# Kernel tuning notes

Measured on AMD Instinct MI355X. Metric: run time of the kernel, lower is better.

## Reference

```python
import jax, jax.numpy as jnp
import numpy as np

H = 8          # multihead_num (also groups of the Conv1d)
LN_EPS = 1e-5  # torch.nn.LayerNorm default


def _gconv(x, w):
    """Grouped Conv1d, kernel=3, stride=1, 'same' reflect padding, no bias.
    x: [B, C_in, L], w: [C_out, C_in//H, K] (torch OIH layout)."""
    xp = jnp.pad(x, ((0, 0), (0, 0), (1, 1)), mode='reflect')
    return jax.lax.conv_general_dilated(
        xp, w, window_strides=(1,), padding='VALID',
        feature_group_count=H, dimension_numbers=('NCH', 'OIH', 'NCH'))


def setup_inputs() -> dict:
    key = jax.random.key(0)
    ks = jax.random.split(key, 5)
    B, C, L = 8, 512, 1024
    q = jax.random.normal(ks[0], (B, C, L), jnp.float32)
    k = jax.random.normal(ks[1], (B, C, L), jnp.float32)
    # causal mask: 1 above the diagonal -> -1e9 subtracted pre-softmax
    mask = jnp.triu(jnp.ones((L, L), jnp.float32), k=1)
    # init_params: std = sqrt(2 / (C_out + C_in/groups))
    std = float(np.sqrt(2.0 / (C + C // H)))
    wq = jax.random.normal(ks[2], (C, C // H, 3), jnp.float32) * std
    wk = jax.random.normal(ks[3], (C, C // H, 3), jnp.float32) * std
    wv = jax.random.normal(ks[4], (C, C // H, 3), jnp.float32) * std
    gamma = jnp.ones((C,), jnp.float32)
    beta = jnp.zeros((C,), jnp.float32)
    return {"q": q, "k": k, "mask": mask, "wq": wq, "wk": wk, "wv": wv,
            "gamma": gamma, "beta": beta}


def reference(q, k, mask, wq, wk, wv, gamma, beta):
    init = q                               # residual branch, [B, C, L]
    B, C, L = q.shape
    D = C // H                             # head dim
    v = k                                  # inputs list of length 2 -> v = k

    qh = _gconv(q, wq).reshape(B, H, D, L)  # split(dim=1)+cat(dim=0) == head axis
    kh = _gconv(k, wk).reshape(B, H, D, L)
    vh = _gconv(v, wv).reshape(B, H, D, L)

    # scores: q^T k per head; NOTE: scaled by sqrt(multihead_num), as in source
    scores = jnp.einsum('bhdl,bhdm->bhlm', qh, kh) / jnp.sqrt(
        jnp.asarray(H, qh.dtype))
    scores = scores - 1e9 * mask           # mask broadcast over [B, H]
    att = jax.nn.softmax(scores, axis=-1)  # dropout p=0.0 -> identity

    # o = att @ v^T, then concat heads along channel (head-major order)
    o = jnp.einsum('bhlm,bhdm->blhd', att, vh).reshape(B, L, C)

    # residual add + LayerNorm over channel dim
    x = o + jnp.swapaxes(init, 1, 2)       # [B, L, C]
    mu = jnp.mean(x, axis=-1, keepdims=True)
    var = jnp.mean(jnp.square(x - mu), axis=-1, keepdims=True)
    y = (x - mu) * jax.lax.rsqrt(var + LN_EPS) * gamma + beta
    return jnp.swapaxes(y, 1, 2)           # [B, C, L]
```

## Files before the change

kernel.cpp:

```cpp
#include <hip/hip_runtime.h>
#include <math.h>

#define H 8
#define B 8
#define C 512
#define L 1024
#define D 64
#define LDK 72

typedef __attribute__((ext_vector_type(4))) float f32x4;
typedef __attribute__((ext_vector_type(8))) short bf16x8;

static __device__ __forceinline__ short f2bf(float x) {
    union { float f; unsigned u; } v; v.f = x;
    unsigned r = v.u + 0x7FFFu + ((v.u >> 16) & 1u);
    return (short)(r >> 16);
}
static __device__ __forceinline__ short f2bf_fast(float x) {
    union { float f; unsigned u; } v; v.f = x;
    return (short)((v.u + 0x8000u) >> 16);
}
static __device__ __forceinline__ int pack2(short a, short b) {
    return (int)((unsigned short)a | ((unsigned)(unsigned short)b << 16));
}
static __device__ __forceinline__ float bfs2f(short v) {
    union { unsigned u; float f; } w; w.u = ((unsigned)(unsigned short)v) << 16;
    return w.f;
}

__global__ __launch_bounds__(256) void wprep_kernel(
    const float* __restrict__ wq, const float* __restrict__ wk,
    const float* __restrict__ wv, short* __restrict__ wtg)
{
    int idx = blockIdx.x * 256 + threadIdx.x;
    int jj    = idx & 7;
    int quad  = (idx >> 3) & 3;
    int d     = (idx >> 5) & 63;
    int r     = idx >> 11;
    int khalf = r & 1;  r >>= 1;
    int t     = r % 3;  r /= 3;
    int h     = r & 7;
    int conv  = r >> 3;
    const float* w = (conv == 0) ? wq : (conv == 1) ? wk : wv;
    int j_in = khalf * 32 + quad * 8 + jj;
    float v = w[(h * 64 + d) * 192 + j_in * 3 + t];
    if (conv == 0) v *= 0.51012254f;
    wtg[idx] = f2bf(v);
}

__global__ __launch_bounds__(256) void conv_kernel(
    const float* __restrict__ q, const float* __restrict__ k,
    const short* __restrict__ wtg,
    short* __restrict__ qh, short* __restrict__ kh, short* __restrict__ vh)
{
    int bx   = blockIdx.x;
    int tile = bx & 15;
    int h    = (bx >> 4) & 7;
    int b    = (bx >> 7) & 7;
    int src  = bx >> 10;

    __shared__ short xT[66 * LDK];

    int l0  = tile * 64;
    int tid = threadIdx.x;
    int wave = tid >> 6, lane = tid & 63;
    int n = lane & 15, quad = lane >> 4;

    const float* x  = src ? k : q;
    const float* xb = x + (size_t)(b * C + h * 64) * L + l0;

    int c0 = src ? 1 : 0;
    const short* wb0 = wtg + (size_t)((c0 * 8 + h) * 3 * 2) * 2048;
    bf16x8 wf[3][2], wf2[3][2];
    #pragma unroll
    for (int t = 0; t < 3; t++)
        #pragma unroll
        for (int kk = 0; kk < 2; kk++)
            wf[t][kk] = *(const bf16x8*)(wb0 + (t * 2 + kk) * 2048
                                         + (wave * 16 + n) * 32 + quad * 8);
    if (src) {
        const short* wb1 = wtg + (size_t)((2 * 8 + h) * 3 * 2) * 2048;
        #pragma unroll
        for (int t = 0; t < 3; t++)
            #pragma unroll
            for (int kk = 0; kk < 2; kk++)
                wf2[t][kk] = *(const bf16x8*)(wb1 + (t * 2 + kk) * 2048
                                              + (wave * 16 + n) * 32 + quad * 8);
    }

    {
        int j = tid >> 2;
        #pragma unroll
        for (int s = 0; s < 4; s++) {
            int i = (tid & 3) + s * 4;
            float4 v = *(const float4*)(xb + j * L + i * 4);
            int p = 1 + i * 4;
            xT[(p + 0) * LDK + j] = f2bf(v.x);
            xT[(p + 1) * LDK + j] = f2bf(v.y);
            xT[(p + 2) * LDK + j] = f2bf(v.z);
            xT[(p + 3) * LDK + j] = f2bf(v.w);
        }
        if (tid < 64) {
            int gl = (l0 == 0) ? 1 : (l0 - 1);
            xT[0 * LDK + tid] = f2bf(x[(size_t)(b * C + h * 64 + tid) * L + gl]);
        } else if (tid < 128) {
            int j2 = tid - 64;
            int gl = (l0 + 64 >= L) ? (L - 2) : (l0 + 64);
            xT[65 * LDK + j2] = f2bf(x[(size_t)(b * C + h * 64 + j2) * L + gl]);
        }
    }
    __syncthreads();

    f32x4 acc[4], acc2[4];
    #pragma unroll
    for (int bl = 0; bl < 4; bl++) {
        acc[bl]  = (f32x4){0.f, 0.f, 0.f, 0.f};
        acc2[bl] = (f32x4){0.f, 0.f, 0.f, 0.f};
    }

    #pragma unroll
    for (int bl = 0; bl < 4; bl++) {
        #pragma unroll
        for (int t = 0; t < 3; t++) {
            #pragma unroll
            for (int kk = 0; kk < 2; kk++) {
                bf16x8 bf = *(const bf16x8*)&xT[(bl * 16 + n + t) * LDK
                                                + kk * 32 + quad * 8];
                acc[bl] = __builtin_amdgcn_mfma_f32_16x16x32_bf16(
                    wf[t][kk], bf, acc[bl], 0, 0, 0);
                if (src)
                    acc2[bl] = __builtin_amdgcn_mfma_f32_16x16x32_bf16(
                        wf2[t][kk], bf, acc2[bl], 0, 0, 0);
            }
        }
    }

    int bhh = b * H + h;
    short* o1 = src ? kh : qh;
    {
        short* ob = o1 + ((size_t)bhh * L + l0) * 64;
        #pragma unroll
        for (int bl = 0; bl < 4; bl++) {
            int lg = bl * 16 + n;
            int2 v;
            v.x = pack2(f2bf(acc[bl][0]), f2bf(acc[bl][1]));
            v.y = pack2(f2bf(acc[bl][2]), f2bf(acc[bl][3]));
            *(int2*)&ob[lg * 64 + wave * 16 + quad * 4] = v;
        }
    }
    if (src) {
        short* ob = vh + (size_t)bhh * 64 * L + l0;
        #pragma unroll
        for (int bl = 0; bl < 4; bl++)
            #pragma unroll
            for (int r = 0; r < 4; r++)
                ob[(wave * 16 + quad * 4 + r) * L + bl * 16 + n] = f2bf(acc2[bl][r]);
    }
}

__global__ __launch_bounds__(256, 4) void flash_kernel(
    const short* __restrict__ qh, const short* __restrict__ kh,
    const short* __restrict__ vh, short* __restrict__ ot)
{
    int bx = blockIdx.x;
    int bh = bx & 63;
    int qt = 15 - (bx >> 6);
    int h  = bh & 7, b = bh >> 3;

    __shared__ short Qs[64 * LDK];
    __shared__ short Ks[64 * LDK];
    __shared__ short Vt[64 * LDK];
    __shared__ short Ps[64 * LDK];

    int tid  = threadIdx.x;
    int wave = tid >> 6, lane = tid & 63;
    int n    = lane & 15, quad = lane >> 4;

    const short* Qg = qh + ((size_t)bh * L + qt * 64) * 64;
    for (int i = tid; i < 512; i += 256) {
        int row = i >> 3, ch = i & 7;
        *(int4*)&Qs[row * LDK + ch * 8] = ((const int4*)Qg)[i];
    }

    const short* Kbase = kh + (size_t)bh * L * 64;
    const short* Vbase = vh + (size_t)bh * 64 * L;
    int r0 = tid >> 3,         ch0 = tid & 7;
    int r1 = (tid + 256) >> 3, ch1 = (tid + 256) & 7;

    int4 kreg0 = ((const int4*)Kbase)[tid];
    int4 kreg1 = ((const int4*)Kbase)[tid + 256];
    int4 vreg0 = *(const int4*)(Vbase + r0 * L + ch0 * 8);
    int4 vreg1 = *(const int4*)(Vbase + r1 * L + ch1 * 8);

    __syncthreads();
    bf16x8 qa0 = *(const bf16x8*)&Qs[(wave * 16 + n) * LDK + quad * 8];
    bf16x8 qa1 = *(const bf16x8*)&Qs[(wave * 16 + n) * LDK + 32 + quad * 8];

    const bf16x8 ones = {16256,16256,16256,16256,16256,16256,16256,16256};

    f32x4 O0 = {0.f,0.f,0.f,0.f}, O1 = O0, O2 = O0, O3 = O0;
    f32x4 Lacc = {0.f,0.f,0.f,0.f};

    for (int kt = 0; kt <= qt; kt++) {
        __syncthreads();
        *(int4*)&Ks[r0 * LDK + ch0 * 8] = kreg0;
        *(int4*)&Ks[r1 * LDK + ch1 * 8] = kreg1;
        *(int4*)&Vt[r0 * LDK + ch0 * 8] = vreg0;
        *(int4*)&Vt[r1 * LDK + ch1 * 8] = vreg1;
        __syncthreads();
        if (kt < qt) {
            const int4* Kg = (const int4*)(Kbase + (size_t)(kt + 1) * 64 * 64);
            kreg0 = Kg[tid]; kreg1 = Kg[tid + 256];
            const short* Vg = Vbase + (kt + 1) * 64;
            vreg0 = *(const int4*)(Vg + r0 * L + ch0 * 8);
            vreg1 = *(const int4*)(Vg + r1 * L + ch1 * 8);
        }

        f32x4 s[4];
        #pragma unroll
        for (int bk = 0; bk < 4; bk++) {
            bf16x8 kb0 = *(const bf16x8*)&Ks[(bk * 16 + n) * LDK + quad * 8];
            bf16x8 kb1 = *(const bf16x8*)&Ks[(bk * 16 + n) * LDK + 32 + quad * 8];
            f32x4 acc = {0.f,0.f,0.f,0.f};
            acc = __builtin_amdgcn_mfma_f32_16x16x32_bf16(qa0, kb0, acc, 0, 0, 0);
            acc = __builtin_amdgcn_mfma_f32_16x16x32_bf16(qa1, kb1, acc, 0, 0, 0);
            s[bk] = acc;
        }

        if (kt == qt) {
            #pragma unroll
            for (int bk = 0; bk < 4; bk++)
                #pragma unroll
                for (int r = 0; r < 4; r++)
                    if (bk * 16 + n > wave * 16 + quad * 4 + r)
                        s[bk][r] = -INFINITY;
        }

        #pragma unroll
        for (int bk = 0; bk < 4; bk++)
            #pragma unroll
            for (int r = 0; r < 4; r++)
                Ps[(wave * 16 + quad * 4 + r) * LDK + bk * 16 + n] =
                    f2bf_fast(__builtin_amdgcn_exp2f(s[bk][r] - 20.f));

        bf16x8 pa0 = *(const bf16x8*)&Ps[(wave * 16 + n) * LDK + quad * 8];
        bf16x8 pa1 = *(const bf16x8*)&Ps[(wave * 16 + n) * LDK + 32 + quad * 8];

        Lacc = __builtin_amdgcn_mfma_f32_16x16x32_bf16(pa0, ones, Lacc, 0, 0, 0);
        Lacc = __builtin_amdgcn_mfma_f32_16x16x32_bf16(pa1, ones, Lacc, 0, 0, 0);

        #pragma unroll
        for (int bk = 0; bk < 4; bk++) {
            bf16x8 v0 = *(const bf16x8*)&Vt[(bk * 16 + n) * LDK + quad * 8];
            bf16x8 v1 = *(const bf16x8*)&Vt[(bk * 16 + n) * LDK + 32 + quad * 8];
            f32x4* Op = (bk == 0) ? &O0 : (bk == 1) ? &O1 : (bk == 2) ? &O2 : &O3;
            *Op = __builtin_amdgcn_mfma_f32_16x16x32_bf16(pa0, v0, *Op, 0, 0, 0);
            *Op = __builtin_amdgcn_mfma_f32_16x16x32_bf16(pa1, v1, *Op, 0, 0, 0);
        }
    }

    float inv[4];
    #pragma unroll
    for (int r = 0; r < 4; r++) inv[r] = 1.f / Lacc[r];

    __syncthreads();
    #pragma unroll
    for (int bk = 0; bk < 4; bk++) {
        f32x4* Op = (bk == 0) ? &O0 : (bk == 1) ? &O1 : (bk == 2) ? &O2 : &O3;
        #pragma unroll
        for (int r = 0; r < 4; r++)
            Ks[(bk * 16 + n) * LDK + wave * 16 + quad * 4 + r] =
                f2bf_fast((*Op)[r] * inv[r]);
    }
    __syncthreads();
    #pragma unroll
    for (int jj = 0; jj < 2; jj++) {
        int i = tid + jj * 256;
        int d = i >> 3, seg = i & 7;
        int4 v = *(const int4*)&Ks[d * LDK + seg * 8];
        *(int4*)(ot + ((size_t)(b * C) + h * 64 + d) * L + qt * 64 + seg * 8) = v;
    }
}

__global__ __launch_bounds__(512) void ln_kernel(
    const short* __restrict__ ot, const float* __restrict__ q,
    const float* __restrict__ gamma, const float* __restrict__ beta,
    float* __restrict__ y)
{
    int bx = blockIdx.x;
    int tile = bx & 31;
    int b = bx >> 5;
    int l0 = tile * 32;
    int tid = threadIdx.x;
    int li_ = tid & 31, cs = tid >> 5;

    __shared__ float sp[16][33], ssp[16][33];
    __shared__ float mu_s[32], rs_s[32];

    size_t base = ((size_t)b * C + cs * 32) * L + l0 + li_;
    const short* otp = ot + base;
    const float* qp  = q + base;

    float s = 0.f, ss = 0.f;
    #pragma unroll 4
    for (int cc = 0; cc < 32; cc++) {
        float x = bfs2f(otp[(size_t)cc * L]) + qp[(size_t)cc * L];
        s += x; ss += x * x;
    }
    sp[cs][li_] = s; ssp[cs][li_] = ss;
    __syncthreads();
    if (tid < 32) {
        float t1 = 0.f, t2 = 0.f;
        #pragma unroll
        for (int j = 0; j < 16; j++) { t1 += sp[j][tid]; t2 += ssp[j][tid]; }
        float mean = t1 * (1.f / 512.f);
        float var  = t2 * (1.f / 512.f) - mean * mean;
        mu_s[tid] = mean;
        rs_s[tid] = rsqrtf(var + 1e-5f);
    }
    __syncthreads();
    float mu = mu_s[li_], rs = rs_s[li_];
    float* yp = y + base;
    #pragma unroll 4
    for (int cc = 0; cc < 32; cc++) {
        int c = cs * 32 + cc;
        float x = bfs2f(otp[(size_t)cc * L]) + qp[(size_t)cc * L];
        yp[(size_t)cc * L] = (x - mu) * rs * gamma[c] + beta[c];
    }
}

extern "C" void kernel_launch(void* const* d_in, const int* in_sizes, int n_in,
                              void* d_out, int out_size, void* d_ws, size_t ws_size,
                              hipStream_t stream)
{
    const float* q     = (const float*)d_in[0];
    const float* k     = (const float*)d_in[1];
    const float* wq    = (const float*)d_in[3];
    const float* wk    = (const float*)d_in[4];
    const float* wv    = (const float*)d_in[5];
    const float* gamma = (const float*)d_in[6];
    const float* beta  = (const float*)d_in[7];
    float* y = (float*)d_out;

    const size_t N = (size_t)B * H * L * D;
    short* qh  = (short*)d_ws;
    short* kh  = qh + N;
    short* vh  = kh + N;
    short* ot  = vh + N;
    short* wtg = ot + N;

    wprep_kernel<<<1152, 256, 0, stream>>>(wq, wk, wv, wtg);
    conv_kernel<<<2 * B * H * (L / 64), 256, 0, stream>>>(q, k, wtg, qh, kh, vh);
    flash_kernel<<<B * H * (L / 64), 256, 0, stream>>>(qh, kh, vh, ot);
    ln_kernel<<<B * (L / 32), 512, 0, stream>>>(ot, q, gamma, beta, y);
}
```

Measured before the change: 140.5 us.

## Tile and swizzle QKV layout, async LDS loads in flash, cache LN inputs

```diff
diff --git a/kernel.cpp b/kernel.cpp
--- a/kernel.cpp
+++ b/kernel.cpp
@@ -26,6 +26,11 @@
 static __device__ __forceinline__ float bfs2f(short v) {
     union { unsigned u; float f; } w; w.u = ((unsigned)(unsigned short)v) << 16;
     return w.f;
+}
+static __device__ __forceinline__ void async16(const void* g, void* s) {
+    __builtin_amdgcn_global_load_lds(
+        (const __attribute__((address_space(1))) int*)g,
+        (__attribute__((address_space(3))) int*)s, 16, 0, 0);
 }
 
 __global__ __launch_bounds__(256) void wprep_kernel(
@@ -138,23 +143,29 @@
     int bhh = b * H + h;
     short* o1 = src ? kh : qh;
     {
-        short* ob = o1 + ((size_t)bhh * L + l0) * 64;
+        short* ob = o1 + ((size_t)(bhh * 16 + tile)) * 4096;
+        int ch = wave * 2 + (quad >> 1);
         #pragma unroll
         for (int bl = 0; bl < 4; bl++) {
-            int lg = bl * 16 + n;
+            int l = bl * 16 + n;
+            int phys = ch ^ (l & 7);
             int2 v;
             v.x = pack2(f2bf(acc[bl][0]), f2bf(acc[bl][1]));
             v.y = pack2(f2bf(acc[bl][2]), f2bf(acc[bl][3]));
-            *(int2*)&ob[lg * 64 + wave * 16 + quad * 4] = v;
+            *(int2*)&ob[l * 64 + phys * 8 + (quad & 1) * 4] = v;
         }
     }
     if (src) {
-        short* ob = vh + (size_t)bhh * 64 * L + l0;
+        short* vb = vh + ((size_t)(bhh * 16 + tile)) * 4096;
         #pragma unroll
         for (int bl = 0; bl < 4; bl++)
             #pragma unroll
-            for (int r = 0; r < 4; r++)
-                ob[(wave * 16 + quad * 4 + r) * L + bl * 16 + n] = f2bf(acc2[bl][r]);
+            for (int r = 0; r < 4; r++) {
+                int d = wave * 16 + quad * 4 + r;
+                int l = bl * 16 + n;
+                int phys = (bl * 2 + (n >> 3)) ^ (d & 7);
+                vb[d * 64 + phys * 8 + (l & 7)] = f2bf(acc2[bl][r]);
+            }
     }
 }
 
@@ -162,39 +173,37 @@
     const short* __restrict__ qh, const short* __restrict__ kh,
     const short* __restrict__ vh, short* __restrict__ ot)
 {
+    __shared__ __align__(16) short lds[20480];
+
     int bx = blockIdx.x;
     int bh = bx & 63;
     int qt = 15 - (bx >> 6);
     int h  = bh & 7, b = bh >> 3;
 
-    __shared__ short Qs[64 * LDK];
-    __shared__ short Ks[64 * LDK];
-    __shared__ short Vt[64 * LDK];
-    __shared__ short Ps[64 * LDK];
-
     int tid  = threadIdx.x;
     int wave = tid >> 6, lane = tid & 63;
     int n    = lane & 15, quad = lane >> 4;
 
-    const short* Qg = qh + ((size_t)bh * L + qt * 64) * 64;
-    for (int i = tid; i < 512; i += 256) {
-        int row = i >> 3, ch = i & 7;
-        *(int4*)&Qs[row * LDK + ch * 8] = ((const int4*)Qg)[i];
-    }
-
-    const short* Kbase = kh + (size_t)bh * L * 64;
-    const short* Vbase = vh + (size_t)bh * 64 * L;
-    int r0 = tid >> 3,         ch0 = tid & 7;
-    int r1 = (tid + 256) >> 3, ch1 = (tid + 256) & 7;
-
-    int4 kreg0 = ((const int4*)Kbase)[tid];
-    int4 kreg1 = ((const int4*)Kbase)[tid + 256];
-    int4 vreg0 = *(const int4*)(Vbase + r0 * L + ch0 * 8);
-    int4 vreg1 = *(const int4*)(Vbase + r1 * L + ch1 * 8);
-
-    __syncthreads();
-    bf16x8 qa0 = *(const bf16x8*)&Qs[(wave * 16 + n) * LDK + quad * 8];
-    bf16x8 qa1 = *(const bf16x8*)&Qs[(wave * 16 + n) * LDK + 32 + quad * 8];
+    const short* Qg    = qh + ((size_t)(bh * 16 + qt)) * 4096;
+    const short* Kbase = kh + (size_t)bh * 65536;
+    const short* Vbase = vh + (size_t)bh * 65536;
+
+    {
+        int ci = wave * 64 + lane;
+        async16((const int4*)Qg + ci,           lds + wave * 512);
+        async16((const int4*)Qg + ci + 256,     lds + 2048 + wave * 512);
+        async16((const int4*)Kbase + ci,        lds + 4096 + wave * 512);
+        async16((const int4*)Kbase + ci + 256,  lds + 4096 + 2048 + wave * 512);
+        async16((const int4*)Vbase + ci,        lds + 8192 + wave * 512);
+        async16((const int4*)Vbase + ci + 256,  lds + 8192 + 2048 + wave * 512);
+    }
+    __syncthreads();
+
+    int ph0 = quad ^ (n & 7);
+    int ph1 = (quad + 4) ^ (n & 7);
+
+    bf16x8 qa0 = *(const bf16x8*)&lds[(wave * 16 + n) * 64 + ph0 * 8];
+    bf16x8 qa1 = *(const bf16x8*)&lds[(wave * 16 + n) * 64 + ph1 * 8];
 
     const bf16x8 ones = {16256,16256,16256,16256,16256,16256,16256,16256};
 
@@ -202,25 +211,26 @@
     f32x4 Lacc = {0.f,0.f,0.f,0.f};
 
     for (int kt = 0; kt <= qt; kt++) {
-        __syncthreads();
-        *(int4*)&Ks[r0 * LDK + ch0 * 8] = kreg0;
-        *(int4*)&Ks[r1 * LDK + ch1 * 8] = kreg1;
-        *(int4*)&Vt[r0 * LDK + ch0 * 8] = vreg0;
-        *(int4*)&Vt[r1 * LDK + ch1 * 8] = vreg1;
-        __syncthreads();
+        if (kt > 0) __syncthreads();
         if (kt < qt) {
-            const int4* Kg = (const int4*)(Kbase + (size_t)(kt + 1) * 64 * 64);
-            kreg0 = Kg[tid]; kreg1 = Kg[tid + 256];
-            const short* Vg = Vbase + (kt + 1) * 64;
-            vreg0 = *(const int4*)(Vg + r0 * L + ch0 * 8);
-            vreg1 = *(const int4*)(Vg + r1 * L + ch1 * 8);
-        }
+            const short* Kg = Kbase + (size_t)(kt + 1) * 4096;
+            const short* Vg = Vbase + (size_t)(kt + 1) * 4096;
+            int koff = 4096 + (((kt + 1) & 1)) * 8192;
+            int ci = wave * 64 + lane;
+            async16((const int4*)Kg + ci,       lds + koff + wave * 512);
+            async16((const int4*)Kg + ci + 256, lds + koff + 2048 + wave * 512);
+            async16((const int4*)Vg + ci,       lds + koff + 4096 + wave * 512);
+            async16((const int4*)Vg + ci + 256, lds + koff + 4096 + 2048 + wave * 512);
+        }
+        const short* Kb = lds + 4096 + (kt & 1) * 8192;
+        const short* Vb = Kb + 4096;
 
         f32x4 s[4];
         #pragma unroll
         for (int bk = 0; bk < 4; bk++) {
-            bf16x8 kb0 = *(const bf16x8*)&Ks[(bk * 16 + n) * LDK + quad * 8];
-            bf16x8 kb1 = *(const bf16x8*)&Ks[(bk * 16 + n) * LDK + 32 + quad * 8];
+            int row = bk * 16 + n;
+            bf16x8 kb0 = *(const bf16x8*)&Kb[row * 64 + ph0 * 8];
+            bf16x8 kb1 = *(const bf16x8*)&Kb[row * 64 + ph1 * 8];
             f32x4 acc = {0.f,0.f,0.f,0.f};
             acc = __builtin_amdgcn_mfma_f32_16x16x32_bf16(qa0, kb0, acc, 0, 0, 0);
             acc = __builtin_amdgcn_mfma_f32_16x16x32_bf16(qa1, kb1, acc, 0, 0, 0);
@@ -239,20 +249,24 @@
         #pragma unroll
         for (int bk = 0; bk < 4; bk++)
             #pragma unroll
-            for (int r = 0; r < 4; r++)
-                Ps[(wave * 16 + quad * 4 + r) * LDK + bk * 16 + n] =
+            for (int r = 0; r < 4; r++) {
+                int prow = wave * 16 + quad * 4 + r;
+                int pch  = (bk * 2 + (n >> 3)) ^ (prow & 7);
+                lds[prow * 64 + pch * 8 + (n & 7)] =
                     f2bf_fast(__builtin_amdgcn_exp2f(s[bk][r] - 20.f));
-
-        bf16x8 pa0 = *(const bf16x8*)&Ps[(wave * 16 + n) * LDK + quad * 8];
-        bf16x8 pa1 = *(const bf16x8*)&Ps[(wave * 16 + n) * LDK + 32 + quad * 8];
+            }
+
+        bf16x8 pa0 = *(const bf16x8*)&lds[(wave * 16 + n) * 64 + ph0 * 8];
+        bf16x8 pa1 = *(const bf16x8*)&lds[(wave * 16 + n) * 64 + ph1 * 8];
 
         Lacc = __builtin_amdgcn_mfma_f32_16x16x32_bf16(pa0, ones, Lacc, 0, 0, 0);
         Lacc = __builtin_amdgcn_mfma_f32_16x16x32_bf16(pa1, ones, Lacc, 0, 0, 0);
 
         #pragma unroll
         for (int bk = 0; bk < 4; bk++) {
-            bf16x8 v0 = *(const bf16x8*)&Vt[(bk * 16 + n) * LDK + quad * 8];
-            bf16x8 v1 = *(const bf16x8*)&Vt[(bk * 16 + n) * LDK + 32 + quad * 8];
+            int row = bk * 16 + n;
+            bf16x8 v0 = *(const bf16x8*)&Vb[row * 64 + ph0 * 8];
+            bf16x8 v1 = *(const bf16x8*)&Vb[row * 64 + ph1 * 8];
             f32x4* Op = (bk == 0) ? &O0 : (bk == 1) ? &O1 : (bk == 2) ? &O2 : &O3;
             *Op = __builtin_amdgcn_mfma_f32_16x16x32_bf16(pa0, v0, *Op, 0, 0, 0);
             *Op = __builtin_amdgcn_mfma_f32_16x16x32_bf16(pa1, v1, *Op, 0, 0, 0);
@@ -264,12 +278,13 @@
     for (int r = 0; r < 4; r++) inv[r] = 1.f / Lacc[r];
 
     __syncthreads();
+    short* Eb = lds + 4096;
     #pragma unroll
     for (int bk = 0; bk < 4; bk++) {
         f32x4* Op = (bk == 0) ? &O0 : (bk == 1) ? &O1 : (bk == 2) ? &O2 : &O3;
         #pragma unroll
         for (int r = 0; r < 4; r++)
-            Ks[(bk * 16 + n) * LDK + wave * 16 + quad * 4 + r] =
+            Eb[(bk * 16 + n) * LDK + wave * 16 + quad * 4 + r] =
                 f2bf_fast((*Op)[r] * inv[r]);
     }
     __syncthreads();
@@ -277,7 +292,7 @@
     for (int jj = 0; jj < 2; jj++) {
         int i = tid + jj * 256;
         int d = i >> 3, seg = i & 7;
-        int4 v = *(const int4*)&Ks[d * LDK + seg * 8];
+        int4 v = *(const int4*)&Eb[d * LDK + seg * 8];
         *(int4*)(ot + ((size_t)(b * C) + h * 64 + d) * L + qt * 64 + seg * 8) = v;
     }
 }
@@ -301,10 +316,12 @@
     const short* otp = ot + base;
     const float* qp  = q + base;
 
+    float xr[32];
     float s = 0.f, ss = 0.f;
-    #pragma unroll 4
+    #pragma unroll
     for (int cc = 0; cc < 32; cc++) {
         float x = bfs2f(otp[(size_t)cc * L]) + qp[(size_t)cc * L];
+        xr[cc] = x;
         s += x; ss += x * x;
     }
     sp[cs][li_] = s; ssp[cs][li_] = ss;
@@ -321,11 +338,10 @@
     __syncthreads();
     float mu = mu_s[li_], rs = rs_s[li_];
     float* yp = y + base;
-    #pragma unroll 4
+    #pragma unroll
     for (int cc = 0; cc < 32; cc++) {
         int c = cs * 32 + cc;
-        float x = bfs2f(otp[(size_t)cc * L]) + qp[(size_t)cc * L];
-        yp[(size_t)cc * L] = (x - mu) * rs * gamma[c] + beta[c];
+        yp[(size_t)cc * L] = (xr[cc] - mu) * rs * gamma[c] + beta[c];
     }
 }
 
```

Result: faster. 135.6 us (-3.5%).
